# Performance work log

Hardware: AMD Instinct MI355X
Metric: run time of the kernel (lower is better)

Reference implementation:

```python
import jax, jax.numpy as jnp
import numpy as np

LEAK = 0.1
EPS = 1e-5

N, C, T, V = 32, 64, 400, 27
S, IC, O = 2, 16, 64  # num_subset, inter_channels, out_channels


def _make_pe(channel, joint_num, time_len):
    pos = np.tile(np.arange(joint_num), time_len).astype(np.float32)[:, None]
    div = np.exp(np.arange(0, channel, 2).astype(np.float32) * (-(np.log(10000.0) / channel)))
    pe = np.zeros((time_len * joint_num, channel), np.float32)
    pe[:, 0::2] = np.sin(pos * div)
    pe[:, 1::2] = np.cos(pos * div)
    # (T*V, C) -> (1, C, T, V)
    return jnp.asarray(pe.reshape(time_len, joint_num, channel).transpose(2, 0, 1)[None])


def setup_inputs() -> dict:
    key = jax.random.key(0)
    ks = jax.random.split(key, 16)
    w = lambda k, shp, fan: jax.random.normal(k, shp, jnp.float32) * (1.0 / np.sqrt(fan))
    inp = {
        "x": jax.random.normal(ks[0], (N, C, T, V), jnp.float32),
        "pe": _make_pe(C, V, T),
        # in_nets: Conv2d(C, 2*S*IC, 1)
        "W_in": w(ks[1], (2 * S * IC, C), C),
        "b_in": jnp.zeros((2 * S * IC,), jnp.float32),
        "alphas": jnp.ones((1, S, 1, 1), jnp.float32),
        "att0": jnp.ones((1, S, V, V), jnp.float32) / V,
        # out_nets: Conv2d(S*C, O, 1) + BN
        "W_out": w(ks[2], (O, S * C), S * C),
        "b_out": jnp.zeros((O,), jnp.float32),
        "g_out": jnp.ones((O,), jnp.float32),
        "be_out": jnp.zeros((O,), jnp.float32),
        "m_out": jax.random.normal(ks[3], (O,), jnp.float32) * 0.1,
        "v_out": jax.random.uniform(ks[4], (O,), jnp.float32, 0.5, 1.5),
        # ff_nets: Conv2d(O, O, 1) + BN
        "W_ff": w(ks[5], (O, O), O),
        "b_ff": jnp.zeros((O,), jnp.float32),
        "g_ff": jnp.ones((O,), jnp.float32),
        "be_ff": jnp.zeros((O,), jnp.float32),
        "m_ff": jax.random.normal(ks[6], (O,), jnp.float32) * 0.1,
        "v_ff": jax.random.uniform(ks[7], (O,), jnp.float32, 0.5, 1.5),
        # out_nett: Conv2d(O, O, (3,1), pad (1,0)) + BN
        "W_t": w(ks[8], (O, O, 3, 1), O * 3),
        "b_t": jnp.zeros((O,), jnp.float32),
        "g_t": jnp.ones((O,), jnp.float32),
        "be_t": jnp.zeros((O,), jnp.float32),
        "m_t": jax.random.normal(ks[9], (O,), jnp.float32) * 0.1,
        "v_t": jax.random.uniform(ks[10], (O,), jnp.float32, 0.5, 1.5),
    }
    return inp


def _lrelu(x):
    return jnp.where(x >= 0, x, LEAK * x)


def _bn(x, g, b, m, v):
    scale = g / jnp.sqrt(v + EPS)
    return (x - m[None, :, None, None]) * scale[None, :, None, None] + b[None, :, None, None]


def _conv1x1(x, W, b):
    return jnp.einsum('oc,nctv->notv', W, x) + b[None, :, None, None]


def reference(x, pe, W_in, b_in, alphas, att0, W_out, b_out, g_out, be_out, m_out, v_out,
              W_ff, b_ff, g_ff, be_ff, m_ff, v_ff, W_t, b_t, g_t, be_t, m_t, v_t):
    n, c, t, v_ = x.shape
    s = alphas.shape[1]
    ic = W_in.shape[0] // (2 * s)
    # positional encoding on the attention-input branch only
    y = x + pe[:, :, :t]
    qk = _conv1x1(y, W_in, b_in).reshape(n, 2 * s, ic, t, v_)
    q, k = qk[:, :s], qk[:, s:]
    # atts buffer is zeros; dropout is identity in eval
    att = jnp.tanh(jnp.einsum('nsctu,nsctv->nsuv', q, k) / (ic * t)) * alphas + att0
    y = jnp.einsum('nctu,nsuv->nsctv', x, att).reshape(n, s * c, t, v_)
    y = _bn(_conv1x1(y, W_out, b_out), g_out, be_out, m_out, v_out)
    y = _lrelu(x + y)  # downs1 = identity
    yf = _bn(_conv1x1(y, W_ff, b_ff), g_ff, be_ff, m_ff, v_ff)
    y = _lrelu(x + yf)  # downs2 = identity
    z = jax.lax.conv_general_dilated(
        y, W_t, window_strides=(1, 1), padding=((1, 1), (0, 0)),
        dimension_numbers=('NCHW', 'OIHW', 'NCHW'))
    z = _bn(z + b_t[None, :, None, None], g_t, be_t, m_t, v_t)
    z = _lrelu(y + z)  # downt2 = identity
    return z
```

## Files before the change

kernel.cpp:

```cpp
#include <hip/hip_runtime.h>
#include <hip/hip_bf16.h>

typedef __hip_bfloat16 bf16;
typedef unsigned short u16;
typedef __attribute__((ext_vector_type(8))) short short8;
typedef __attribute__((ext_vector_type(4))) short s4v;
typedef __attribute__((ext_vector_type(4))) float f32x4;
typedef __attribute__((ext_vector_type(4))) unsigned int u32x4;

#define LEAK 0.1f
#define EPS_ 1e-5f
#define MFMA(a, b, c) __builtin_amdgcn_mfma_f32_16x16x32_bf16(a, b, c, 0, 0, 0)

__device__ __forceinline__ float u2f(u16 u) { return __uint_as_float(((unsigned int)u) << 16); }
__device__ __forceinline__ u16 f2u(float f) {
  bf16 h = __float2bfloat16(f);
  u16 r;
  __builtin_memcpy(&r, &h, 2);
  return r;
}
__device__ __forceinline__ f32x4 z4() { f32x4 z = {0.f, 0.f, 0.f, 0.f}; return z; }

__global__ __launch_bounds__(256) void g_qk(
    const float* __restrict__ x, const float* __restrict__ pe,
    const float* __restrict__ W_in, const float* __restrict__ b_in,
    u16* __restrict__ qG, u16* __restrict__ kG)
{
  __shared__ u32x4 sB[16][2][64];
  const int tid = threadIdx.x;
  const int w = tid >> 6, lane = tid & 63;
  const int m = lane & 15, quad = lane >> 4;
  const int n = blockIdx.y, p0 = blockIdx.x * 256;

  short8 aW[2];
#pragma unroll
  for (int kf = 0; kf < 2; ++kf) {
    short8 tt;
#pragma unroll
    for (int j = 0; j < 8; ++j)
      tt[j] = (short)f2u(W_in[(16 * w + m) * 64 + 32 * kf + 8 * quad + j]);
    aW[kf] = tt;
  }
  float bb[4];
#pragma unroll
  for (int r = 0; r < 4; ++r) bb[r] = b_in[16 * w + quad * 4 + r];

#pragma unroll
  for (int k = 0; k < 8; ++k) {
    int slot = tid + 256 * k;
    int tile = slot >> 7, kf = (slot >> 6) & 1;
    int qq = (slot >> 4) & 3, mm = slot & 15;
    int p = p0 + tile * 16 + mm;
    int c0 = kf * 32 + qq * 8;
    short8 tt = {0, 0, 0, 0, 0, 0, 0, 0};
    if (p < 10800) {
#pragma unroll
      for (int j = 0; j < 8; ++j)
        tt[j] = (short)f2u(x[(n * 64 + c0 + j) * 10800 + p] +
                           pe[(c0 + j) * 10800 + p]);
    }
    *(short8*)&sB[tile][kf][slot & 63] = tt;
  }
  __syncthreads();

  u16* dst = (w < 2 ? qG : kG) + (n * 2 + (w & 1)) * 32 * 6400;
#pragma unroll 4
  for (int tile = 0; tile < 16; ++tile) {
    short8 b0 = *(const short8*)&sB[tile][0][lane];
    short8 b1 = *(const short8*)&sB[tile][1][lane];
    f32x4 acc = MFMA(aW[0], b0, z4());
    acc = MFMA(aW[1], b1, acc);
    int p = p0 + tile * 16 + m;
    if (p < 10800) {
      unsigned t = (unsigned)p / 27u;
      unsigned u = (unsigned)p - 27u * t;
      s4v pk;
#pragma unroll
      for (int reg = 0; reg < 4; ++reg) pk[reg] = (short)f2u(acc[reg] + bb[reg]);
      *(s4v*)&dst[(u * 400 + t) * 16 + quad * 4] = pk;
    }
  }
}

__global__ __launch_bounds__(256) void g_att(
    const u16* __restrict__ qG, const u16* __restrict__ kG,
    const float* __restrict__ alphas, const float* __restrict__ att0,
    float* __restrict__ att)
{
  __shared__ float sred[4][64][16];
  const int tid = threadIdx.x;
  const int w = tid >> 6, lane = tid & 63;
  const int m = lane & 15, quad = lane >> 4;
  const int s = blockIdx.x, n = blockIdx.y;
  const u16* qb = qG + (n * 2 + s) * 32 * 6400;
  const u16* kb = kG + (n * 2 + s) * 32 * 6400;

  f32x4 a00 = z4(), a01 = z4(), a10 = z4(), a11 = z4();
#pragma unroll 2
  for (int it = 0; it < 25; ++it) {
    int kk0 = w * 1600 + it * 64;
#pragma unroll
    for (int kf = 0; kf < 2; ++kf) {
      int kk = kk0 + kf * 32 + quad * 8;
      short8 aq0 = *(const short8*)&qb[m * 6400 + kk];
      short8 aq1 = *(const short8*)&qb[(16 + m) * 6400 + kk];
      short8 bk0 = *(const short8*)&kb[m * 6400 + kk];
      short8 bk1 = *(const short8*)&kb[(16 + m) * 6400 + kk];
      a00 = MFMA(aq0, bk0, a00);
      a01 = MFMA(aq0, bk1, a01);
      a10 = MFMA(aq1, bk0, a10);
      a11 = MFMA(aq1, bk1, a11);
    }
  }
  *(f32x4*)&sred[w][lane][0] = a00;
  *(f32x4*)&sred[w][lane][4] = a01;
  *(f32x4*)&sred[w][lane][8] = a10;
  *(f32x4*)&sred[w][lane][12] = a11;
  __syncthreads();
  const float al = alphas[s];
#pragma unroll
  for (int k = 0; k < 4; ++k) {
    int slot = tid + 256 * k;
    int lsrc = slot >> 4, idx = slot & 15;
    float val = sred[0][lsrc][idx] + sred[1][lsrc][idx] +
                sred[2][lsrc][idx] + sred[3][lsrc][idx];
    int f = idx >> 2, reg = idx & 3;
    int ut = f >> 1, vt = f & 1;
    int qq = lsrc >> 4, mm = lsrc & 15;
    int u = ut * 16 + qq * 4 + reg, v = vt * 16 + mm;
    if (u < 27 && v < 27)
      att[(n * 2 + s) * 729 + u * 27 + v] =
          tanhf(val * (1.f / 6400.f)) * al + att0[s * 729 + u * 27 + v];
  }
}

__global__ __launch_bounds__(256) void g_ab(
    const float* __restrict__ x, const float* __restrict__ att,
    const float* __restrict__ W_out, const float* __restrict__ b_out,
    const float* __restrict__ g_out, const float* __restrict__ be_out,
    const float* __restrict__ m_out, const float* __restrict__ v_out,
    u16* __restrict__ y3T)
{
  __shared__ u32x4 sy2f[4][2][4][64];
  const int tid = threadIdx.x;
  const int w = tid >> 6, lane = tid & 63;
  const int m = lane & 15, quad = lane >> 4;
  const int n = blockIdx.y, t0 = blockIdx.x * 4;

  short8 bAtt[4];
#pragma unroll
  for (int s = 0; s < 2; ++s)
#pragma unroll
    for (int nt = 0; nt < 2; ++nt) {
      short8 tt;
#pragma unroll
      for (int j = 0; j < 8; ++j) {
        int u = 8 * quad + j, v = 16 * nt + m;
        tt[j] = (u < 27 && v < 27) ? (short)f2u(att[(n * 2 + s) * 729 + u * 27 + v]) : (short)0;
      }
      bAtt[s * 2 + nt] = tt;
    }
  short8 aWo[4];
#pragma unroll
  for (int kf = 0; kf < 4; ++kf) {
    short8 tt;
#pragma unroll
    for (int j = 0; j < 8; ++j)
      tt[j] = (short)f2u(W_out[(16 * w + m) * 128 + 32 * kf + 8 * quad + j]);
    aWo[kf] = tt;
  }
  float Ao[4], Bo[4];
#pragma unroll
  for (int reg = 0; reg < 4; ++reg) {
    int o = 16 * w + quad * 4 + reg;
    float sc = g_out[o] * rsqrtf(v_out[o] + EPS_);
    Ao[reg] = sc;
    Bo[reg] = (b_out[o] - m_out[o]) * sc + be_out[o];
  }

  const int q1 = quad & 1;
  const int qp = (2 * w + (quad >> 1)) & 3;
#pragma unroll
  for (int tc = 0; tc < 4; ++tc) {
    int t = t0 + tc;
    short8 ax;
#pragma unroll
    for (int j = 0; j < 8; ++j) {
      int u = quad * 8 + j;
      ax[j] = (u < 27) ? (short)f2u(x[((n * 64 + 16 * w + m) * 400 + t) * 27 + u]) : (short)0;
    }
    f32x4 acc[4];
#pragma unroll
    for (int f = 0; f < 4; ++f) acc[f] = MFMA(ax, bAtt[f], z4());
#pragma unroll
    for (int s = 0; s < 2; ++s)
#pragma unroll
      for (int nt = 0; nt < 2; ++nt) {
        f32x4 a = acc[s * 2 + nt];
        s4v pk;
#pragma unroll
        for (int reg = 0; reg < 4; ++reg) pk[reg] = (short)f2u(a[reg]);
        int kfp = 2 * s + (w >> 1);
        *(s4v*)((u16*)&sy2f[tc][nt][kfp][qp * 16 + m] + 4 * q1) = pk;
      }
  }
  __syncthreads();
#pragma unroll
  for (int tc = 0; tc < 4; ++tc) {
    int t = t0 + tc;
#pragma unroll
    for (int vt = 0; vt < 2; ++vt) {
      f32x4 a0 = z4();
#pragma unroll
      for (int kf = 0; kf < 4; ++kf) {
        short8 b = *(const short8*)&sy2f[tc][vt][kf][lane];
        a0 = MFMA(aWo[kf], b, a0);
      }
      int v = vt * 16 + m;
      if (v < 27) {
        s4v pk;
#pragma unroll
        for (int reg = 0; reg < 4; ++reg) {
          int o = 16 * w + quad * 4 + reg;
          float r = x[((n * 64 + o) * 400 + t) * 27 + v] + a0[reg] * Ao[reg] + Bo[reg];
          pk[reg] = (short)f2u((r >= 0.f) ? r : LEAK * r);
        }
        *(s4v*)&y3T[(unsigned)(n * 10800 + t * 27 + v) * 64 + 16 * w + quad * 4] = pk;
      }
    }
  }
}

__global__ __launch_bounds__(256) void g_cd(
    const float* __restrict__ x, const u16* __restrict__ y3T,
    const float* __restrict__ W_ff, const float* __restrict__ b_ff,
    const float* __restrict__ g_ff, const float* __restrict__ be_ff,
    const float* __restrict__ m_ff, const float* __restrict__ v_ff,
    const float* __restrict__ W_t, const float* __restrict__ b_t,
    const float* __restrict__ g_t, const float* __restrict__ be_t,
    const float* __restrict__ m_t, const float* __restrict__ v_t,
    float* __restrict__ out)
{
  __shared__ u32x4 sy4f[6][2][2][64];
  const int tid = threadIdx.x;
  const int w = tid >> 6, lane = tid & 63;
  const int m = lane & 15, quad = lane >> 4;
  const int n = blockIdx.y, t0 = blockIdx.x * 4;

  short8 aWf[2], aWt[6];
#pragma unroll
  for (int kf = 0; kf < 2; ++kf) {
    short8 tt;
#pragma unroll
    for (int j = 0; j < 8; ++j)
      tt[j] = (short)f2u(W_ff[(16 * w + m) * 64 + 32 * kf + 8 * quad + j]);
    aWf[kf] = tt;
  }
#pragma unroll
  for (int kf = 0; kf < 6; ++kf) {
    short8 tt;
    int dt = kf >> 1;
#pragma unroll
    for (int j = 0; j < 8; ++j) {
      int ii = 32 * (kf & 1) + 8 * quad + j;
      tt[j] = (short)f2u(W_t[((16 * w + m) * 64 + ii) * 3 + dt]);
    }
    aWt[kf] = tt;
  }
  float Af[4], Bf[4], At[4], Bt[4];
#pragma unroll
  for (int reg = 0; reg < 4; ++reg) {
    int o = 16 * w + quad * 4 + reg;
    float sc;
    sc = g_ff[o] * rsqrtf(v_ff[o] + EPS_); Af[reg] = sc; Bf[reg] = (b_ff[o] - m_ff[o]) * sc + be_ff[o];
    sc = g_t[o] * rsqrtf(v_t[o] + EPS_);   At[reg] = sc; Bt[reg] = (b_t[o] - m_t[o]) * sc + be_t[o];
  }

  const int q1 = quad & 1;
  const int qp = (2 * w + (quad >> 1)) & 3;
  const int kfp = w >> 1;
  f32x4 y4res[4][2];
#pragma unroll
  for (int tl = 0; tl < 6; ++tl) {
    int t = t0 - 1 + tl;
    if (t >= 0 && t < 400) {
#pragma unroll
      for (int vt = 0; vt < 2; ++vt) {
        int v = vt * 16 + m;
        unsigned p = (unsigned)(n * 10800 + t * 27 + v);
        f32x4 acc = z4();
#pragma unroll
        for (int kf = 0; kf < 2; ++kf) {
          short8 b = *(const short8*)&y3T[p * 64 + kf * 32 + quad * 8];
          acc = MFMA(aWf[kf], b, acc);
        }
        s4v pk;
        f32x4 yr;
#pragma unroll
        for (int reg = 0; reg < 4; ++reg) {
          int o = 16 * w + quad * 4 + reg;
          float xr = (v < 27) ? x[((n * 64 + o) * 400 + t) * 27 + v] : 0.f;
          float r = xr + acc[reg] * Af[reg] + Bf[reg];
          r = (r >= 0.f) ? r : LEAK * r;
          yr[reg] = r;
          pk[reg] = (short)f2u(r);
        }
        if (tl >= 1 && tl <= 4) y4res[tl - 1][vt] = yr;
        *(s4v*)((u16*)&sy4f[tl][vt][kfp][qp * 16 + m] + 4 * q1) = pk;
      }
    } else {
      s4v zz = {0, 0, 0, 0};
#pragma unroll
      for (int vt = 0; vt < 2; ++vt) {
        if (tl >= 1 && tl <= 4) y4res[tl - 1][vt] = z4();
        *(s4v*)((u16*)&sy4f[tl][vt][kfp][qp * 16 + m] + 4 * q1) = zz;
      }
    }
  }
  __syncthreads();
#pragma unroll
  for (int tc = 0; tc < 4; ++tc) {
    int t = t0 + tc;
#pragma unroll
    for (int vt = 0; vt < 2; ++vt) {
      f32x4 acc = z4();
#pragma unroll
      for (int kf = 0; kf < 6; ++kf) {
        short8 b = *(const short8*)&sy4f[tc + (kf >> 1)][vt][kf & 1][lane];
        acc = MFMA(aWt[kf], b, acc);
      }
      int v = vt * 16 + m;
      if (v < 27) {
#pragma unroll
        for (int reg = 0; reg < 4; ++reg) {
          int o = 16 * w + quad * 4 + reg;
          float r = y4res[tc][vt][reg] + acc[reg] * At[reg] + Bt[reg];
          out[((n * 64 + o) * 400 + t) * 27 + v] = (r >= 0.f) ? r : LEAK * r;
        }
      }
    }
  }
}

extern "C" void kernel_launch(void* const* d_in, const int* in_sizes, int n_in,
                              void* d_out, int out_size, void* d_ws, size_t ws_size,
                              hipStream_t stream)
{
  const float* x      = (const float*)d_in[0];
  const float* pe     = (const float*)d_in[1];
  const float* W_in   = (const float*)d_in[2];
  const float* b_in   = (const float*)d_in[3];
  const float* alphas = (const float*)d_in[4];
  const float* att0   = (const float*)d_in[5];
  const float* W_out  = (const float*)d_in[6];
  const float* b_out  = (const float*)d_in[7];
  const float* g_out  = (const float*)d_in[8];
  const float* be_out = (const float*)d_in[9];
  const float* m_out  = (const float*)d_in[10];
  const float* v_out  = (const float*)d_in[11];
  const float* W_ff   = (const float*)d_in[12];
  const float* b_ff   = (const float*)d_in[13];
  const float* g_ff   = (const float*)d_in[14];
  const float* be_ff  = (const float*)d_in[15];
  const float* m_ff   = (const float*)d_in[16];
  const float* v_ff   = (const float*)d_in[17];
  const float* W_t    = (const float*)d_in[18];
  const float* b_t    = (const float*)d_in[19];
  const float* g_t    = (const float*)d_in[20];
  const float* be_t   = (const float*)d_in[21];
  const float* m_t    = (const float*)d_in[22];
  const float* v_t    = (const float*)d_in[23];

  float* att = (float*)d_ws;
  u16* qG  = (u16*)((char*)d_ws + (1u << 20));
  u16* kG  = (u16*)((char*)d_ws + (1u << 20) + 26214400u);
  u16* y3T = (u16*)((char*)d_ws + (1u << 20));

  g_qk<<<dim3(43, 32), 256, 0, stream>>>(x, pe, W_in, b_in, qG, kG);
  g_att<<<dim3(2, 32), 256, 0, stream>>>(qG, kG, alphas, att0, att);
  g_ab<<<dim3(100, 32), 256, 0, stream>>>(
      x, att, W_out, b_out, g_out, be_out, m_out, v_out, y3T);
  g_cd<<<dim3(100, 32), 256, 0, stream>>>(
      x, y3T, W_ff, b_ff, g_ff, be_ff, m_ff, v_ff,
      W_t, b_t, g_t, be_t, m_t, v_t, (float*)d_out);
}
```

Baseline: 462.6 us.

## Split attention reduction across blocks with atomics and widen kernels to 512 threads

The QK-attention reduction used to run as one block per (s,n), only 64 blocks in total. It is now split into 25 K-chunks per (s,n), which write partial sums through atomicAdd into a memset buffer. A separate finalize kernel then applies tanh, alpha and att0. The qk, ab and cd kernels now use 512-thread blocks, with two wave groups sharing the per-block work. The cd kernel handles 8 time steps per block, which cuts halo recomputation, and it reads the residual back from bf16 shared memory instead of holding it in fp32 registers. That last change lowers register pressure but makes the residual less precise, and the atomics and extra launches add overhead.

After: 429.6 us. -7.1%, faster.

```diff
diff --git a/kernel.cpp b/kernel.cpp
--- a/kernel.cpp
+++ b/kernel.cpp
@@ -21,7 +21,7 @@
 }
 __device__ __forceinline__ f32x4 z4() { f32x4 z = {0.f, 0.f, 0.f, 0.f}; return z; }
 
-__global__ __launch_bounds__(256) void g_qk(
+__global__ __launch_bounds__(512, 4) void g_qk(
     const float* __restrict__ x, const float* __restrict__ pe,
     const float* __restrict__ W_in, const float* __restrict__ b_in,
     u16* __restrict__ qG, u16* __restrict__ kG)
@@ -30,6 +30,7 @@
   const int tid = threadIdx.x;
   const int w = tid >> 6, lane = tid & 63;
   const int m = lane & 15, quad = lane >> 4;
+  const int ot = w & 3, g = w >> 2;
   const int n = blockIdx.y, p0 = blockIdx.x * 256;
 
   short8 aW[2];
@@ -38,16 +39,16 @@
     short8 tt;
 #pragma unroll
     for (int j = 0; j < 8; ++j)
-      tt[j] = (short)f2u(W_in[(16 * w + m) * 64 + 32 * kf + 8 * quad + j]);
+      tt[j] = (short)f2u(W_in[(16 * ot + m) * 64 + 32 * kf + 8 * quad + j]);
     aW[kf] = tt;
   }
   float bb[4];
 #pragma unroll
-  for (int r = 0; r < 4; ++r) bb[r] = b_in[16 * w + quad * 4 + r];
-
-#pragma unroll
-  for (int k = 0; k < 8; ++k) {
-    int slot = tid + 256 * k;
+  for (int r = 0; r < 4; ++r) bb[r] = b_in[16 * ot + quad * 4 + r];
+
+#pragma unroll
+  for (int k = 0; k < 4; ++k) {
+    int slot = tid + 512 * k;
     int tile = slot >> 7, kf = (slot >> 6) & 1;
     int qq = (slot >> 4) & 3, mm = slot & 15;
     int p = p0 + tile * 16 + mm;
@@ -63,9 +64,10 @@
   }
   __syncthreads();
 
-  u16* dst = (w < 2 ? qG : kG) + (n * 2 + (w & 1)) * 32 * 6400;
+  u16* dst = (ot < 2 ? qG : kG) + (n * 2 + (ot & 1)) * 32 * 6400;
 #pragma unroll 4
-  for (int tile = 0; tile < 16; ++tile) {
+  for (int ti = 0; ti < 8; ++ti) {
+    int tile = 8 * g + ti;
     short8 b0 = *(const short8*)&sB[tile][0][lane];
     short8 b1 = *(const short8*)&sB[tile][1][lane];
     f32x4 acc = MFMA(aW[0], b0, z4());
@@ -82,42 +84,38 @@
   }
 }
 
-__global__ __launch_bounds__(256) void g_att(
+__global__ __launch_bounds__(256) void g_att_part(
     const u16* __restrict__ qG, const u16* __restrict__ kG,
-    const float* __restrict__ alphas, const float* __restrict__ att0,
     float* __restrict__ att)
 {
   __shared__ float sred[4][64][16];
   const int tid = threadIdx.x;
   const int w = tid >> 6, lane = tid & 63;
   const int m = lane & 15, quad = lane >> 4;
-  const int s = blockIdx.x, n = blockIdx.y;
+  const int s = blockIdx.x / 25, kc = blockIdx.x % 25;
+  const int n = blockIdx.y;
   const u16* qb = qG + (n * 2 + s) * 32 * 6400;
   const u16* kb = kG + (n * 2 + s) * 32 * 6400;
 
   f32x4 a00 = z4(), a01 = z4(), a10 = z4(), a11 = z4();
-#pragma unroll 2
-  for (int it = 0; it < 25; ++it) {
-    int kk0 = w * 1600 + it * 64;
-#pragma unroll
-    for (int kf = 0; kf < 2; ++kf) {
-      int kk = kk0 + kf * 32 + quad * 8;
-      short8 aq0 = *(const short8*)&qb[m * 6400 + kk];
-      short8 aq1 = *(const short8*)&qb[(16 + m) * 6400 + kk];
-      short8 bk0 = *(const short8*)&kb[m * 6400 + kk];
-      short8 bk1 = *(const short8*)&kb[(16 + m) * 6400 + kk];
-      a00 = MFMA(aq0, bk0, a00);
-      a01 = MFMA(aq0, bk1, a01);
-      a10 = MFMA(aq1, bk0, a10);
-      a11 = MFMA(aq1, bk1, a11);
-    }
+  const int kk0 = kc * 256 + w * 64;
+#pragma unroll
+  for (int kf = 0; kf < 2; ++kf) {
+    int kk = kk0 + kf * 32 + quad * 8;
+    short8 aq0 = *(const short8*)&qb[m * 6400 + kk];
+    short8 aq1 = *(const short8*)&qb[(16 + m) * 6400 + kk];
+    short8 bk0 = *(const short8*)&kb[m * 6400 + kk];
+    short8 bk1 = *(const short8*)&kb[(16 + m) * 6400 + kk];
+    a00 = MFMA(aq0, bk0, a00);
+    a01 = MFMA(aq0, bk1, a01);
+    a10 = MFMA(aq1, bk0, a10);
+    a11 = MFMA(aq1, bk1, a11);
   }
   *(f32x4*)&sred[w][lane][0] = a00;
   *(f32x4*)&sred[w][lane][4] = a01;
   *(f32x4*)&sred[w][lane][8] = a10;
   *(f32x4*)&sred[w][lane][12] = a11;
   __syncthreads();
-  const float al = alphas[s];
 #pragma unroll
   for (int k = 0; k < 4; ++k) {
     int slot = tid + 256 * k;
@@ -129,12 +127,22 @@
     int qq = lsrc >> 4, mm = lsrc & 15;
     int u = ut * 16 + qq * 4 + reg, v = vt * 16 + mm;
     if (u < 27 && v < 27)
-      att[(n * 2 + s) * 729 + u * 27 + v] =
-          tanhf(val * (1.f / 6400.f)) * al + att0[s * 729 + u * 27 + v];
-  }
-}
-
-__global__ __launch_bounds__(256) void g_ab(
+      atomicAdd(&att[(n * 2 + s) * 729 + u * 27 + v], val);
+  }
+}
+
+__global__ __launch_bounds__(256) void k_att_fin(
+    float* __restrict__ att, const float* __restrict__ alphas,
+    const float* __restrict__ att0)
+{
+  int i = blockIdx.x * 256 + threadIdx.x;
+  if (i >= 32 * 2 * 729) return;
+  int s = (i / 729) & 1;
+  int r = i % 729;
+  att[i] = tanhf(att[i] * (1.f / 6400.f)) * alphas[s] + att0[s * 729 + r];
+}
+
+__global__ __launch_bounds__(512, 4) void g_ab(
     const float* __restrict__ x, const float* __restrict__ att,
     const float* __restrict__ W_out, const float* __restrict__ b_out,
     const float* __restrict__ g_out, const float* __restrict__ be_out,
@@ -145,6 +153,7 @@
   const int tid = threadIdx.x;
   const int w = tid >> 6, lane = tid & 63;
   const int m = lane & 15, quad = lane >> 4;
+  const int ot = w & 3, g = w >> 2;
   const int n = blockIdx.y, t0 = blockIdx.x * 4;
 
   short8 bAtt[4];
@@ -166,28 +175,29 @@
     short8 tt;
 #pragma unroll
     for (int j = 0; j < 8; ++j)
-      tt[j] = (short)f2u(W_out[(16 * w + m) * 128 + 32 * kf + 8 * quad + j]);
+      tt[j] = (short)f2u(W_out[(16 * ot + m) * 128 + 32 * kf + 8 * quad + j]);
     aWo[kf] = tt;
   }
   float Ao[4], Bo[4];
 #pragma unroll
   for (int reg = 0; reg < 4; ++reg) {
-    int o = 16 * w + quad * 4 + reg;
+    int o = 16 * ot + quad * 4 + reg;
     float sc = g_out[o] * rsqrtf(v_out[o] + EPS_);
     Ao[reg] = sc;
     Bo[reg] = (b_out[o] - m_out[o]) * sc + be_out[o];
   }
 
   const int q1 = quad & 1;
-  const int qp = (2 * w + (quad >> 1)) & 3;
-#pragma unroll
-  for (int tc = 0; tc < 4; ++tc) {
+  const int qp = (2 * ot + (quad >> 1)) & 3;
+#pragma unroll
+  for (int li = 0; li < 2; ++li) {
+    int tc = 2 * li + g;
     int t = t0 + tc;
     short8 ax;
 #pragma unroll
     for (int j = 0; j < 8; ++j) {
       int u = quad * 8 + j;
-      ax[j] = (u < 27) ? (short)f2u(x[((n * 64 + 16 * w + m) * 400 + t) * 27 + u]) : (short)0;
+      ax[j] = (u < 27) ? (short)f2u(x[((n * 64 + 16 * ot + m) * 400 + t) * 27 + u]) : (short)0;
     }
     f32x4 acc[4];
 #pragma unroll
@@ -200,13 +210,14 @@
         s4v pk;
 #pragma unroll
         for (int reg = 0; reg < 4; ++reg) pk[reg] = (short)f2u(a[reg]);
-        int kfp = 2 * s + (w >> 1);
+        int kfp = 2 * s + (ot >> 1);
         *(s4v*)((u16*)&sy2f[tc][nt][kfp][qp * 16 + m] + 4 * q1) = pk;
       }
   }
   __syncthreads();
 #pragma unroll
-  for (int tc = 0; tc < 4; ++tc) {
+  for (int ci = 0; ci < 2; ++ci) {
+    int tc = 2 * ci + g;
     int t = t0 + tc;
 #pragma unroll
     for (int vt = 0; vt < 2; ++vt) {
@@ -221,17 +232,17 @@
         s4v pk;
 #pragma unroll
         for (int reg = 0; reg < 4; ++reg) {
-          int o = 16 * w + quad * 4 + reg;
+          int o = 16 * ot + quad * 4 + reg;
           float r = x[((n * 64 + o) * 400 + t) * 27 + v] + a0[reg] * Ao[reg] + Bo[reg];
           pk[reg] = (short)f2u((r >= 0.f) ? r : LEAK * r);
         }
-        *(s4v*)&y3T[(unsigned)(n * 10800 + t * 27 + v) * 64 + 16 * w + quad * 4] = pk;
-      }
-    }
-  }
-}
-
-__global__ __launch_bounds__(256) void g_cd(
+        *(s4v*)&y3T[(unsigned)(n * 10800 + t * 27 + v) * 64 + 16 * ot + quad * 4] = pk;
+      }
+    }
+  }
+}
+
+__global__ __launch_bounds__(512, 4) void g_cd(
     const float* __restrict__ x, const u16* __restrict__ y3T,
     const float* __restrict__ W_ff, const float* __restrict__ b_ff,
     const float* __restrict__ g_ff, const float* __restrict__ be_ff,
@@ -241,11 +252,12 @@
     const float* __restrict__ m_t, const float* __restrict__ v_t,
     float* __restrict__ out)
 {
-  __shared__ u32x4 sy4f[6][2][2][64];
+  __shared__ u32x4 sy4f[10][2][2][64];
   const int tid = threadIdx.x;
   const int w = tid >> 6, lane = tid & 63;
   const int m = lane & 15, quad = lane >> 4;
-  const int n = blockIdx.y, t0 = blockIdx.x * 4;
+  const int ot = w & 3, g = w >> 2;
+  const int n = blockIdx.y, t0 = blockIdx.x * 8;
 
   short8 aWf[2], aWt[6];
 #pragma unroll
@@ -253,7 +265,7 @@
     short8 tt;
 #pragma unroll
     for (int j = 0; j < 8; ++j)
-      tt[j] = (short)f2u(W_ff[(16 * w + m) * 64 + 32 * kf + 8 * quad + j]);
+      tt[j] = (short)f2u(W_ff[(16 * ot + m) * 64 + 32 * kf + 8 * quad + j]);
     aWf[kf] = tt;
   }
 #pragma unroll
@@ -263,25 +275,25 @@
 #pragma unroll
     for (int j = 0; j < 8; ++j) {
       int ii = 32 * (kf & 1) + 8 * quad + j;
-      tt[j] = (short)f2u(W_t[((16 * w + m) * 64 + ii) * 3 + dt]);
+      tt[j] = (short)f2u(W_t[((16 * ot + m) * 64 + ii) * 3 + dt]);
     }
     aWt[kf] = tt;
   }
   float Af[4], Bf[4], At[4], Bt[4];
 #pragma unroll
   for (int reg = 0; reg < 4; ++reg) {
-    int o = 16 * w + quad * 4 + reg;
+    int o = 16 * ot + quad * 4 + reg;
     float sc;
     sc = g_ff[o] * rsqrtf(v_ff[o] + EPS_); Af[reg] = sc; Bf[reg] = (b_ff[o] - m_ff[o]) * sc + be_ff[o];
     sc = g_t[o] * rsqrtf(v_t[o] + EPS_);   At[reg] = sc; Bt[reg] = (b_t[o] - m_t[o]) * sc + be_t[o];
   }
 
   const int q1 = quad & 1;
-  const int qp = (2 * w + (quad >> 1)) & 3;
-  const int kfp = w >> 1;
-  f32x4 y4res[4][2];
-#pragma unroll
-  for (int tl = 0; tl < 6; ++tl) {
+  const int qp = (2 * ot + (quad >> 1)) & 3;
+  const int kfp = ot >> 1;
+#pragma unroll
+  for (int li = 0; li < 5; ++li) {
+    int tl = 2 * li + g;
     int t = t0 - 1 + tl;
     if (t >= 0 && t < 400) {
 #pragma unroll
@@ -295,31 +307,26 @@
           acc = MFMA(aWf[kf], b, acc);
         }
         s4v pk;
-        f32x4 yr;
 #pragma unroll
         for (int reg = 0; reg < 4; ++reg) {
-          int o = 16 * w + quad * 4 + reg;
+          int o = 16 * ot + quad * 4 + reg;
           float xr = (v < 27) ? x[((n * 64 + o) * 400 + t) * 27 + v] : 0.f;
           float r = xr + acc[reg] * Af[reg] + Bf[reg];
-          r = (r >= 0.f) ? r : LEAK * r;
-          yr[reg] = r;
-          pk[reg] = (short)f2u(r);
+          pk[reg] = (short)f2u((r >= 0.f) ? r : LEAK * r);
         }
-        if (tl >= 1 && tl <= 4) y4res[tl - 1][vt] = yr;
         *(s4v*)((u16*)&sy4f[tl][vt][kfp][qp * 16 + m] + 4 * q1) = pk;
       }
     } else {
       s4v zz = {0, 0, 0, 0};
 #pragma unroll
-      for (int vt = 0; vt < 2; ++vt) {
-        if (tl >= 1 && tl <= 4) y4res[tl - 1][vt] = z4();
+      for (int vt = 0; vt < 2; ++vt)
         *(s4v*)((u16*)&sy4f[tl][vt][kfp][qp * 16 + m] + 4 * q1) = zz;
-      }
     }
   }
   __syncthreads();
 #pragma unroll
-  for (int tc = 0; tc < 4; ++tc) {
+  for (int ci = 0; ci < 4; ++ci) {
+    int tc = 2 * ci + g;
     int t = t0 + tc;
 #pragma unroll
     for (int vt = 0; vt < 2; ++vt) {
@@ -331,10 +338,11 @@
       }
       int v = vt * 16 + m;
       if (v < 27) {
+        s4v res = *(const s4v*)((const u16*)&sy4f[tc + 1][vt][kfp][qp * 16 + m] + 4 * q1);
 #pragma unroll
         for (int reg = 0; reg < 4; ++reg) {
-          int o = 16 * w + quad * 4 + reg;
-          float r = y4res[tc][vt][reg] + acc[reg] * At[reg] + Bt[reg];
+          int o = 16 * ot + quad * 4 + reg;
+          float r = u2f((u16)res[reg]) + acc[reg] * At[reg] + Bt[reg];
           out[((n * 64 + o) * 400 + t) * 27 + v] = (r >= 0.f) ? r : LEAK * r;
         }
       }
@@ -376,11 +384,13 @@
   u16* kG  = (u16*)((char*)d_ws + (1u << 20) + 26214400u);
   u16* y3T = (u16*)((char*)d_ws + (1u << 20));
 
-  g_qk<<<dim3(43, 32), 256, 0, stream>>>(x, pe, W_in, b_in, qG, kG);
-  g_att<<<dim3(2, 32), 256, 0, stream>>>(qG, kG, alphas, att0, att);
-  g_ab<<<dim3(100, 32), 256, 0, stream>>>(
+  hipMemsetAsync(att, 0, 32 * 2 * 729 * sizeof(float), stream);
+  g_qk<<<dim3(43, 32), 512, 0, stream>>>(x, pe, W_in, b_in, qG, kG);
+  g_att_part<<<dim3(50, 32), 256, 0, stream>>>(qG, kG, att);
+  k_att_fin<<<dim3(183), 256, 0, stream>>>(att, alphas, att0);
+  g_ab<<<dim3(100, 32), 512, 0, stream>>>(
       x, att, W_out, b_out, g_out, be_out, m_out, v_out, y3T);
-  g_cd<<<dim3(100, 32), 256, 0, stream>>>(
+  g_cd<<<dim3(50, 32), 512, 0, stream>>>(
       x, y3T, W_ff, b_ff, g_ff, be_ff, m_ff, v_ff,
       W_t, b_t, g_t, be_t, m_t, v_t, (float*)d_out);
 }
```
